# Optimization experiments

Hardware: AMD Instinct MI355X
Metric: run time of the kernel (lower is better)

The kernel has to match this reference:

```python
import jax, jax.numpy as jnp
from jax import lax
import numpy as np

DN = ('NDHWC', 'DHWIO', 'NDHWC')

def _conv(x, W):
    # stride-1 kernel-3 sparse conv on dense grid: SAME conv; absent voxels are zero
    return lax.conv_general_dilated(x, W, (1, 1, 1), 'SAME', dimension_numbers=DN)

def _tconv(x, W):
    # kernel-2 stride-2 generative transpose conv: exactly doubles each spatial dim
    return lax.conv_transpose(x, W, (2, 2, 2), 'VALID', dimension_numbers=DN)

def _pool(h):
    B, D1, D2, D3, C = h.shape
    return h.reshape(B, D1 // 2, 2, D2 // 2, 2, D3 // 2, 2, C).max(axis=(2, 4, 6))

def _pool_mask(m):
    B, D1, D2, D3 = m.shape
    return m.reshape(B, D1 // 2, 2, D2 // 2, 2, D3 // 2, 2).max(axis=(2, 4, 6))

def _up_mask(m):
    return jnp.repeat(jnp.repeat(jnp.repeat(m, 2, axis=1), 2, axis=2), 2, axis=3)

def setup_inputs() -> dict:
    key = jax.random.key(0)
    ks = jax.random.split(key, 6)
    B, G = 2, 128
    x = jax.random.normal(ks[0], (B, G, G, G, 1), dtype=jnp.float32)
    occ = jax.random.randint(ks[1], (B, G, G, G), 0, 10, dtype=jnp.int32)
    def xavier(k, shape):
        fan_in = np.prod(shape[:-1]); fan_out = shape[-1]
        std = np.sqrt(2.0 / (fan_in + fan_out)).astype(np.float32)
        return jax.random.normal(k, shape, dtype=jnp.float32) * std
    W1 = xavier(ks[2], (3, 3, 3, 1, 16))
    W2 = xavier(ks[3], (3, 3, 3, 16, 4))
    Wt1 = xavier(ks[4], (2, 2, 2, 4, 16))
    Wt2 = xavier(ks[5], (2, 2, 2, 16, 1))
    return {"x": x, "W1": W1, "W2": W2, "Wt1": Wt1, "Wt2": Wt2, "occ": occ}

def reference(x, W1, W2, Wt1, Wt2, occ):
    m0 = (occ == 0).astype(x.dtype)            # occupancy mask at full res
    xm = x * m0[..., None]
    h = jax.nn.relu(_conv(xm, W1)) * m0[..., None]   # coords unchanged
    h = _pool(h); m1 = _pool_mask(m0)                # stride-2 max pool on sparse coords
    h = jax.nn.relu(_conv(h, W2)) * m1[..., None]
    h = _pool(h); m2 = _pool_mask(m1)
    m3 = _up_mask(m2)                                # transpose conv emits all children coords
    h = jax.nn.relu(_tconv(h, Wt1)) * m3[..., None]
    m4 = _up_mask(m3)
    out = jax.nn.sigmoid(_tconv(h, Wt2)) * m4[..., None]
    return out
```

## Files before the change

### kernel.cpp

```cpp
#include <hip/hip_runtime.h>
#include <hip/hip_fp16.h>

#define G 128

typedef _Float16 h2_t __attribute__((ext_vector_type(2)));

union U16 { uint4 u; h2_t h2[4]; };
union HV  { uint4 u; h2_t h2[4]; };
union PK2 { uint2 u; h2_t h[2]; };

__device__ __forceinline__ float dot2f(h2_t a, h2_t b, float c) {
#if __has_builtin(__builtin_amdgcn_fdot2)
    return __builtin_amdgcn_fdot2(a, b, c, false);
#else
    return c + (float)a.x * (float)b.x + (float)a.y * (float)b.y;
#endif
}

__device__ __forceinline__ float dot4(float4 a, float4 b) {
    return a.x * b.x + a.y * b.y + a.z * b.z + a.w * b.w;
}

__global__ __launch_bounds__(256, 1)
void k_conv1_pool(const float* __restrict__ x, const int* __restrict__ occ,
                  const float* __restrict__ W1,
                  __half* __restrict__ h1p, float* __restrict__ m1)
{
    __shared__ __align__(16) _Float16      sx[10 * 18 * 24];
    __shared__ __align__(16) int           pacc[16 * 256];
    __shared__ __align__(4)  unsigned short slist[2048];
    __shared__ __align__(16) h2_t          w1L[216];
    __shared__ __align__(4)  unsigned char sm1[256];
    __shared__ int                         scnt;

    const int bx = blockIdx.x, by = blockIdx.y;
    const int b  = blockIdx.z >> 4, zt = blockIdx.z & 15;
    const int tid = threadIdx.x;

    const int z0 = zt * 8 - 1, y0 = by * 16 - 1;
    const int base_b = b * G * G * G;

    int4   ro[5];
    float4 rx[5];
    #pragma unroll
    for (int it = 0; it < 5; ++it) {
        int c = it * 256 + tid;
        int cc = c < 1080 ? c : 1079;
        int row = cc / 6, seg = cc - row * 6;
        int lz  = row / 18, ly = row - lz * 18;
        int gz = z0 + lz, gy = y0 + ly;
        int gxc = (bx << 4) - 4 + (seg << 2);
        bool inb = (unsigned)gz < 128u && (unsigned)gy < 128u && (unsigned)gxc < 128u;
        int gi = inb ? base_b + (gz * G + gy) * G + gxc : base_b;
        ro[it] = *(const int4*)(occ + gi);
        rx[it] = *(const float4*)(x + gi);
    }

    if (tid == 0) scnt = 0;
    {
        uint4 z4 = make_uint4(0u, 0u, 0u, 0u);
        uint4* p4 = (uint4*)pacc;
        p4[tid] = z4; p4[tid + 256] = z4; p4[tid + 512] = z4; p4[tid + 768] = z4;
    }
    if (tid < 64) ((unsigned*)sm1)[tid] = 0u;
    if (tid < 216) {
        float2 f = ((const float2*)W1)[tid];
        h2_t w; w.x = (_Float16)f.x; w.y = (_Float16)f.y;
        w1L[tid] = w;
    }
    __syncthreads();

    #pragma unroll
    for (int it = 0; it < 5; ++it) {
        int c = it * 256 + tid;
        if (c < 1080) {
            int row = c / 6, seg = c - row * 6;
            int lz  = row / 18, ly = row - lz * 18;
            int gz = z0 + lz, gy = y0 + ly;
            int gxc = (bx << 4) - 4 + (seg << 2);
            bool inb = (unsigned)gz < 128u && (unsigned)gy < 128u && (unsigned)gxc < 128u;
            int4   o4 = ro[it];
            float4 x4 = rx[it];
            if (!inb) o4 = make_int4(1, 1, 1, 1);
            h2_t p01, p23;
            p01.x = (o4.x == 0) ? (_Float16)x4.x : (_Float16)0.f;
            p01.y = (o4.y == 0) ? (_Float16)x4.y : (_Float16)0.f;
            p23.x = (o4.z == 0) ? (_Float16)x4.z : (_Float16)0.f;
            p23.y = (o4.w == 0) ? (_Float16)x4.w : (_Float16)0.f;
            PK2 pk; pk.h[0] = p01; pk.h[1] = p23;
            *(uint2*)&sx[row * 24 + (seg << 2)] = pk.u;

            if ((unsigned)(lz - 1) < 8u && (unsigned)(ly - 1) < 16u &&
                (unsigned)(seg - 1) < 4u) {
                int mb = (o4.x == 0 ? 1 : 0) | (o4.y == 0 ? 2 : 0) |
                         (o4.z == 0 ? 4 : 0) | (o4.w == 0 ? 8 : 0);
                if (mb) {
                    int cnt  = __popc(mb);
                    int base = atomicAdd(&scnt, cnt);
                    int cz = lz - 1, cy = ly - 1, cx0v = (seg << 2) - 4;
                    int cellb = (cz >> 1) * 64 + (cy >> 1) * 8;
                    #pragma unroll
                    for (int j = 0; j < 4; ++j) {
                        if (mb & (1 << j)) {
                            slist[base++] = (unsigned short)((cz << 8) | (cy << 4) | (cx0v + j));
                            sm1[cellb + ((cx0v + j) >> 1)] = (unsigned char)1;
                        }
                    }
                }
            }
        }
    }
    __syncthreads();

    const int n = scnt;

    const h2_t zero = (h2_t)(_Float16)0.f;
    for (int kb = 0; kb < n; kb += 256) {
        const int idx = kb + tid;
        if (idx < n) {
            const int code = slist[idx];
            const int cz = code >> 8, cy = (code >> 4) & 15, cx = code & 15;
            const int sb = ((cz + 1) * 18 + (cy + 1)) * 24 + cx + 4;
            h2_t acc[8];
            #pragma unroll
            for (int c = 0; c < 8; ++c) acc[c] = zero;
            #pragma unroll
            for (int kz = 0; kz < 3; ++kz)
            #pragma unroll
            for (int ky = 0; ky < 3; ++ky)
            #pragma unroll
            for (int kx = 0; kx < 3; ++kx) {
                _Float16 v = sx[sb + (kz - 1) * 432 + (ky - 1) * 24 + (kx - 1)];
                h2_t v2 = {v, v};
                const h2_t* w = &w1L[((kz * 3 + ky) * 3 + kx) * 8];
                #pragma unroll
                for (int c = 0; c < 8; ++c) acc[c] = v2 * w[c] + acc[c];
            }
            const int cell = (cz >> 1) * 64 + (cy >> 1) * 8 + (cx >> 1);
            #pragma unroll
            for (int c = 0; c < 8; ++c) {
                atomicMax(&pacc[(2 * c) * 256 + cell],
                          __float_as_int(fmaxf((float)acc[c].x, 0.f)));
                atomicMax(&pacc[(2 * c + 1) * 256 + cell],
                          __float_as_int(fmaxf((float)acc[c].y, 0.f)));
            }
        }
    }
    __syncthreads();

    const int tx = tid & 7, ty = (tid >> 3) & 7, tz = tid >> 6;
    const int pz = zt * 4 + tz, py = by * 8 + ty, px = bx * 8 + tx;
    const int vidx = ((b * 64 + pz) * 64 + py) * 64 + px;
    HV p0, p1;
    #pragma unroll
    for (int c = 0; c < 4; ++c) {
        h2_t a, bq;
        a.x  = (_Float16)__int_as_float(pacc[(2 * c) * 256 + tid]);
        a.y  = (_Float16)__int_as_float(pacc[(2 * c + 1) * 256 + tid]);
        bq.x = (_Float16)__int_as_float(pacc[(8 + 2 * c) * 256 + tid]);
        bq.y = (_Float16)__int_as_float(pacc[(9 + 2 * c) * 256 + tid]);
        p0.h2[c] = a; p1.h2[c] = bq;
    }
    uint4* o = (uint4*)&h1p[(size_t)vidx * 16];
    o[0] = p0.u;
    o[1] = p1.u;
    m1[vidx] = sm1[tid] ? 1.f : 0.f;
}

__global__ __launch_bounds__(256)
void k_conv2_dec(const __half* __restrict__ h1p, const float* __restrict__ m1,
                 const float* __restrict__ W2,
                 const float* __restrict__ Wt1, const float* __restrict__ Wt2,
                 float* __restrict__ out)
{
    __shared__ uint4  tile[1320];
    __shared__ float4 wt1[128];
    __shared__ float4 wt2[32];
    __shared__ __align__(16) h2_t w2L[864];
    __shared__ int    pacc[128];
    __shared__ int    pm[32];
    __shared__ unsigned char slist[256];
    __shared__ int    scnt;

    const int bx = blockIdx.x, by = blockIdx.y;
    const int b  = blockIdx.z >> 4, bz = blockIdx.z & 15;
    const int tid = threadIdx.x;

    const int z0 = bz * 4 - 1, y0 = by * 8 - 1, x0 = bx * 8 - 1;

    uint4 ra[3], rb4[3];
    #pragma unroll
    for (int it = 0; it < 3; ++it) {
        int g = it * 256 + tid;
        int gg = g < 660 ? g : 659;
        int z = gg / 110, r = gg - z * 110, y = r / 11, xx = r - y * 11;
        int gz = z0 + z, gy = y0 + y, gx = x0 + xx;
        bool inb = (unsigned)gz < 64u && (unsigned)gy < 64u && (unsigned)gx < 64u;
        size_t vi = inb ? (size_t)(((b * 64 + gz) * 64 + gy) * 64 + gx) : 0;
        const uint4* src = (const uint4*)&h1p[vi * 16];
        ra[it]  = src[0];
        rb4[it] = src[1];
    }

    const int cx_ = tid & 7, cy_ = (tid >> 3) & 7, cz_ = tid >> 6;
    const float mv = m1[((b * 64 + (bz * 4 + cz_)) * 64 + (by * 8 + cy_)) * 64
                        + (bx * 8 + cx_)];

    if (tid == 0) scnt = 0;
    if (tid < 128) { wt1[tid] = ((const float4*)Wt1)[tid]; pacc[tid] = 0; }
    if (tid < 32)  { wt2[tid] = ((const float4*)Wt2)[tid]; pm[tid] = 0; }
    #pragma unroll
    for (int it = 0; it < 4; ++it) {
        int i = it * 256 + tid;
        if (i < 864) {
            int t = i >> 5, rr = i & 31, co = rr >> 3, p = rr & 7;
            h2_t w;
            w.x = (_Float16)W2[t * 64 + (2 * p) * 4 + co];
            w.y = (_Float16)W2[t * 64 + (2 * p + 1) * 4 + co];
            w2L[i] = w;
        }
    }
    __syncthreads();

    #pragma unroll
    for (int it = 0; it < 3; ++it) {
        int g = it * 256 + tid;
        if (g < 660) {
            int z = g / 110, r = g - z * 110, y = r / 11, xx = r - y * 11;
            int gz = z0 + z, gy = y0 + y, gx = x0 + xx;
            bool inb = (unsigned)gz < 64u && (unsigned)gy < 64u && (unsigned)gx < 64u;
            uint4 a0 = ra[it], a1 = rb4[it];
            if (!inb) { a0 = make_uint4(0u, 0u, 0u, 0u); a1 = a0; }
            tile[g]       = a0;
            tile[660 + g] = a1;
        }
    }
    {
        const int lane = tid & 63;
        bool act = (mv != 0.f);
        unsigned long long bal = __ballot(act);
        int wtot = __popcll(bal);
        int wbase = 0;
        if (lane == 0 && wtot) wbase = atomicAdd(&scnt, wtot);
        wbase = __shfl(wbase, 0);
        if (act) {
            int pre = __popcll(bal & ((1ull << lane) - 1ull));
            slist[wbase + pre] = (unsigned char)tid;
            pm[(cz_ >> 1) * 16 + (cy_ >> 1) * 4 + (cx_ >> 1)] = 1;
        }
    }
    __syncthreads();

    const int n = scnt;

    if (tid < n) {
        const int code = slist[tid];
        const int cx = code & 7, cy = (code >> 3) & 7, cz = code >> 6;
        float acc[4] = {0.f, 0.f, 0.f, 0.f};
        #pragma unroll
        for (int kz = 0; kz < 3; ++kz)
        #pragma unroll
        for (int ky = 0; ky < 3; ++ky) {
            const int rb = ((cz + kz) * 10 + (cy + ky)) * 11 + cx;
            h2_t hp[2][3][4];
            #pragma unroll
            for (int hh = 0; hh < 2; ++hh)
            #pragma unroll
            for (int xi = 0; xi < 3; ++xi) {
                U16 a; a.u = tile[hh * 660 + rb + xi];
                #pragma unroll
                for (int p = 0; p < 4; ++p) hp[hh][xi][p] = a.h2[p];
            }
            const int t3 = (kz * 3 + ky) * 3;
            #pragma unroll
            for (int kx = 0; kx < 3; ++kx) {
                const h2_t* w = &w2L[(t3 + kx) * 32];
                #pragma unroll
                for (int co = 0; co < 4; ++co) {
                    float a = acc[co];
                    #pragma unroll
                    for (int hh = 0; hh < 2; ++hh)
                    #pragma unroll
                    for (int p = 0; p < 4; ++p)
                        a = dot2f(hp[hh][kx][p], w[co * 8 + 4 * hh + p], a);
                    acc[co] = a;
                }
            }
        }
        const int parent = (cz >> 1) * 16 + (cy >> 1) * 4 + (cx >> 1);
        #pragma unroll
        for (int co = 0; co < 4; ++co)
            atomicMax(&pacc[co * 32 + parent],
                      __float_as_int(fmaxf(acc[co], 0.f)));
    }
    __syncthreads();

    {
        const int p  = tid >> 3;
        const int a  = (tid >> 2) & 1;
        const int bb = (tid >> 1) & 1;
        const int e  = tid & 1;
        const int pZ = p >> 4, pY = (p >> 2) & 3, pq = p & 3;
        const int pz = bz * 2 + pZ, py = by * 4 + pY, pxq = bx * 4 + pq;

        const float mm = pm[p] ? 1.f : 0.f;
        const float4 hv = make_float4(__int_as_float(pacc[p]),
                                      __int_as_float(pacc[32 + p]),
                                      __int_as_float(pacc[64 + p]),
                                      __int_as_float(pacc[96 + p]));

        const int b0q = ((((1 - a) * 2 + (1 - bb)) * 2) + 1) * 16;
        const int b1q = ((((1 - a) * 2 + (1 - bb)) * 2) + 0) * 16;
        float4 t0q[4], t1q[4];
        #pragma unroll
        for (int q = 0; q < 4; ++q) {
            float4 a0 = wt1[b0q + q],      a1 = wt1[b0q + 4 + q];
            float4 a2 = wt1[b0q + 8 + q],  a3 = wt1[b0q + 12 + q];
            float4 c0 = wt1[b1q + q],      c1 = wt1[b1q + 4 + q];
            float4 c2 = wt1[b1q + 8 + q],  c3 = wt1[b1q + 12 + q];
            float4 s0, s1;
            s0.x = hv.x * a0.x + hv.y * a1.x + hv.z * a2.x + hv.w * a3.x;
            s0.y = hv.x * a0.y + hv.y * a1.y + hv.z * a2.y + hv.w * a3.y;
            s0.z = hv.x * a0.z + hv.y * a1.z + hv.z * a2.z + hv.w * a3.z;
            s0.w = hv.x * a0.w + hv.y * a1.w + hv.z * a2.w + hv.w * a3.w;
            s1.x = hv.x * c0.x + hv.y * c1.x + hv.z * c2.x + hv.w * c3.x;
            s1.y = hv.x * c0.y + hv.y * c1.y + hv.z * c2.y + hv.w * c3.y;
            s1.z = hv.x * c0.z + hv.y * c1.z + hv.z * c2.z + hv.w * c3.z;
            s1.w = hv.x * c0.w + hv.y * c1.w + hv.z * c2.w + hv.w * c3.w;
            t0q[q] = make_float4(fmaxf(s0.x, 0.f), fmaxf(s0.y, 0.f),
                                 fmaxf(s0.z, 0.f), fmaxf(s0.w, 0.f));
            t1q[q] = make_float4(fmaxf(s1.x, 0.f), fmaxf(s1.y, 0.f),
                                 fmaxf(s1.z, 0.f), fmaxf(s1.w, 0.f));
        }

        const int d = 4 * pz + 2 * a + e;
        #pragma unroll
        for (int f = 0; f < 2; ++f) {
            const int hh = 4 * py + 2 * bb + f;
            const int be = ((1 - e) * 2 + (1 - f)) * 2;
            const float4* wg0 = &wt2[(be + 1) * 4];
            const float4* wg1 = &wt2[(be + 0) * 4];
            float s00 = dot4(t0q[0], wg0[0]) + dot4(t0q[1], wg0[1])
                      + dot4(t0q[2], wg0[2]) + dot4(t0q[3], wg0[3]);
            float s01 = dot4(t0q[0], wg1[0]) + dot4(t0q[1], wg1[1])
                      + dot4(t0q[2], wg1[2]) + dot4(t0q[3], wg1[3]);
            float s10 = dot4(t1q[0], wg0[0]) + dot4(t1q[1], wg0[1])
                      + dot4(t1q[2], wg0[2]) + dot4(t1q[3], wg0[3]);
            float s11 = dot4(t1q[0], wg1[0]) + dot4(t1q[1], wg1[1])
                      + dot4(t1q[2], wg1[2]) + dot4(t1q[3], wg1[3]);
            float4 o;
            o.x = mm / (1.f + __expf(-s00));
            o.y = mm / (1.f + __expf(-s01));
            o.z = mm / (1.f + __expf(-s10));
            o.w = mm / (1.f + __expf(-s11));
            *(float4*)&out[((b * G + d) * G + hh) * G + 4 * pxq] = o;
        }
    }
}

extern "C" void kernel_launch(void* const* d_in, const int* in_sizes, int n_in,
                              void* d_out, int out_size, void* d_ws, size_t ws_size,
                              hipStream_t stream) {
    (void)in_sizes; (void)n_in; (void)out_size; (void)ws_size;
    const float* x   = (const float*)d_in[0];
    const float* W1  = (const float*)d_in[1];
    const float* W2  = (const float*)d_in[2];
    const float* Wt1 = (const float*)d_in[3];
    const float* Wt2 = (const float*)d_in[4];
    const int*   occ = (const int*)d_in[5];
    float* out = (float*)d_out;

    char* ws = (char*)d_ws;
    __half* h1p = (__half*)ws;
    float*  m1  = (float*)(ws + 8388608ull * sizeof(__half));

    k_conv1_pool<<<dim3(8, 8, 32), dim3(256), 0, stream>>>(x, occ, W1, h1p, m1);
    k_conv2_dec<<<dim3(8, 8, 32), dim3(256), 0, stream>>>(h1p, m1, W2, Wt1, Wt2, out);
}
```

Baseline: 152.5 us.

## Halve z-tile per block in both kernels to double grid size

Both kernels now cover half as many z slices per block, so the grid doubles from 2048 to 4096 blocks and shared memory per block shrinks. Conv1 drops the launch-bounds occupancy hint and the register prefetch of occ/x, loading them inline instead. The decoder remaps threads so each one writes a single output row instead of looping over two. The aim is more blocks and higher occupancy to hide latency, at the cost of a larger relative halo overhead (6/4 z rows in conv1, 4/2 in conv2) and half-idle threads in the final write phases.

```diff
diff --git a/kernel.cpp b/kernel.cpp
--- a/kernel.cpp
+++ b/kernel.cpp
@@ -21,48 +21,32 @@
     return a.x * b.x + a.y * b.y + a.z * b.z + a.w * b.w;
 }
 
-__global__ __launch_bounds__(256, 1)
+__global__ __launch_bounds__(256)
 void k_conv1_pool(const float* __restrict__ x, const int* __restrict__ occ,
                   const float* __restrict__ W1,
                   __half* __restrict__ h1p, float* __restrict__ m1)
 {
-    __shared__ __align__(16) _Float16      sx[10 * 18 * 24];
-    __shared__ __align__(16) int           pacc[16 * 256];
-    __shared__ __align__(4)  unsigned short slist[2048];
-    __shared__ __align__(16) h2_t          w1L[216];
-    __shared__ __align__(4)  unsigned char sm1[256];
-    __shared__ int                         scnt;
+    __shared__ __align__(16) _Float16       sx[6 * 18 * 24];
+    __shared__ __align__(16) int            pacc[16 * 128];
+    __shared__ __align__(4)  unsigned short slist[1024];
+    __shared__ __align__(16) h2_t           w1L[216];
+    __shared__ __align__(4)  unsigned char  sm1[128];
+    __shared__ int                          scnt;
 
     const int bx = blockIdx.x, by = blockIdx.y;
-    const int b  = blockIdx.z >> 4, zt = blockIdx.z & 15;
+    const int b  = blockIdx.z >> 5, bz4 = blockIdx.z & 31;
     const int tid = threadIdx.x;
 
-    const int z0 = zt * 8 - 1, y0 = by * 16 - 1;
+    const int z0 = bz4 * 4 - 1, y0 = by * 16 - 1;
     const int base_b = b * G * G * G;
-
-    int4   ro[5];
-    float4 rx[5];
-    #pragma unroll
-    for (int it = 0; it < 5; ++it) {
-        int c = it * 256 + tid;
-        int cc = c < 1080 ? c : 1079;
-        int row = cc / 6, seg = cc - row * 6;
-        int lz  = row / 18, ly = row - lz * 18;
-        int gz = z0 + lz, gy = y0 + ly;
-        int gxc = (bx << 4) - 4 + (seg << 2);
-        bool inb = (unsigned)gz < 128u && (unsigned)gy < 128u && (unsigned)gxc < 128u;
-        int gi = inb ? base_b + (gz * G + gy) * G + gxc : base_b;
-        ro[it] = *(const int4*)(occ + gi);
-        rx[it] = *(const float4*)(x + gi);
-    }
 
     if (tid == 0) scnt = 0;
     {
         uint4 z4 = make_uint4(0u, 0u, 0u, 0u);
-        uint4* p4 = (uint4*)pacc;
-        p4[tid] = z4; p4[tid + 256] = z4; p4[tid + 512] = z4; p4[tid + 768] = z4;
-    }
-    if (tid < 64) ((unsigned*)sm1)[tid] = 0u;
+        ((uint4*)pacc)[tid]       = z4;
+        ((uint4*)pacc)[tid + 256] = z4;
+    }
+    if (tid < 32) ((unsigned*)sm1)[tid] = 0u;
     if (tid < 216) {
         float2 f = ((const float2*)W1)[tid];
         h2_t w; w.x = (_Float16)f.x; w.y = (_Float16)f.y;
@@ -71,16 +55,16 @@
     __syncthreads();
 
     #pragma unroll
-    for (int it = 0; it < 5; ++it) {
+    for (int it = 0; it < 3; ++it) {
         int c = it * 256 + tid;
-        if (c < 1080) {
+        if (c < 648) {
             int row = c / 6, seg = c - row * 6;
-            int lz  = row / 18, ly = row - lz * 18;
-            int gz = z0 + lz, gy = y0 + ly;
-            int gxc = (bx << 4) - 4 + (seg << 2);
+            int lz = row / 18, ly = row - lz * 18;
+            int gz = z0 + lz, gy = y0 + ly, gxc = (bx << 4) - 4 + (seg << 2);
             bool inb = (unsigned)gz < 128u && (unsigned)gy < 128u && (unsigned)gxc < 128u;
-            int4   o4 = ro[it];
-            float4 x4 = rx[it];
+            int gi = inb ? base_b + (gz * G + gy) * G + gxc : base_b;
+            int4   o4 = *(const int4*)(occ + gi);
+            float4 x4 = *(const float4*)(x + gi);
             if (!inb) o4 = make_int4(1, 1, 1, 1);
             h2_t p01, p23;
             p01.x = (o4.x == 0) ? (_Float16)x4.x : (_Float16)0.f;
@@ -90,20 +74,22 @@
             PK2 pk; pk.h[0] = p01; pk.h[1] = p23;
             *(uint2*)&sx[row * 24 + (seg << 2)] = pk.u;
 
-            if ((unsigned)(lz - 1) < 8u && (unsigned)(ly - 1) < 16u &&
-                (unsigned)(seg - 1) < 4u) {
-                int mb = (o4.x == 0 ? 1 : 0) | (o4.y == 0 ? 2 : 0) |
-                         (o4.z == 0 ? 4 : 0) | (o4.w == 0 ? 8 : 0);
+            if ((unsigned)(lz - 1) < 4u && (unsigned)(ly - 1) < 16u) {
+                const int lx0 = seg << 2;
+                int mb = 0;
+                if (o4.x == 0 && (unsigned)(lx0 + 0 - 4) < 16u) mb |= 1;
+                if (o4.y == 0 && (unsigned)(lx0 + 1 - 4) < 16u) mb |= 2;
+                if (o4.z == 0 && (unsigned)(lx0 + 2 - 4) < 16u) mb |= 4;
+                if (o4.w == 0 && (unsigned)(lx0 + 3 - 4) < 16u) mb |= 8;
                 if (mb) {
-                    int cnt  = __popc(mb);
-                    int base = atomicAdd(&scnt, cnt);
-                    int cz = lz - 1, cy = ly - 1, cx0v = (seg << 2) - 4;
-                    int cellb = (cz >> 1) * 64 + (cy >> 1) * 8;
+                    int base = atomicAdd(&scnt, __popc(mb));
+                    const int tb = ((lz - 1) >> 1) * 64 + ((ly - 1) >> 1) * 8;
                     #pragma unroll
                     for (int j = 0; j < 4; ++j) {
                         if (mb & (1 << j)) {
-                            slist[base++] = (unsigned short)((cz << 8) | (cy << 4) | (cx0v + j));
-                            sm1[cellb + ((cx0v + j) >> 1)] = (unsigned char)1;
+                            const int lxv = lx0 + j;
+                            slist[base++] = (unsigned short)((lz << 10) | (ly << 5) | lxv);
+                            sm1[tb + ((lxv - 4) >> 1)] = (unsigned char)1;
                         }
                     }
                 }
@@ -114,57 +100,61 @@
 
     const int n = scnt;
 
-    const h2_t zero = (h2_t)(_Float16)0.f;
-    for (int kb = 0; kb < n; kb += 256) {
-        const int idx = kb + tid;
-        if (idx < n) {
-            const int code = slist[idx];
-            const int cz = code >> 8, cy = (code >> 4) & 15, cx = code & 15;
-            const int sb = ((cz + 1) * 18 + (cy + 1)) * 24 + cx + 4;
-            h2_t acc[8];
-            #pragma unroll
-            for (int c = 0; c < 8; ++c) acc[c] = zero;
-            #pragma unroll
-            for (int kz = 0; kz < 3; ++kz)
-            #pragma unroll
-            for (int ky = 0; ky < 3; ++ky)
-            #pragma unroll
-            for (int kx = 0; kx < 3; ++kx) {
-                _Float16 v = sx[sb + (kz - 1) * 432 + (ky - 1) * 24 + (kx - 1)];
-                h2_t v2 = {v, v};
-                const h2_t* w = &w1L[((kz * 3 + ky) * 3 + kx) * 8];
-                #pragma unroll
-                for (int c = 0; c < 8; ++c) acc[c] = v2 * w[c] + acc[c];
+    {
+        const h2_t zero = (h2_t)(_Float16)0.f;
+        for (int kb = 0; kb < n; kb += 256) {
+            const int idx = kb + tid;
+            if (idx < n) {
+                const int e  = slist[idx];
+                const int lx = e & 31, ly = (e >> 5) & 31, lz = e >> 10;
+                const int sb = (lz * 18 + ly) * 24 + lx;
+                h2_t acc[8];
+                #pragma unroll
+                for (int c = 0; c < 8; ++c) acc[c] = zero;
+                #pragma unroll
+                for (int kz = 0; kz < 3; ++kz)
+                #pragma unroll
+                for (int ky = 0; ky < 3; ++ky)
+                #pragma unroll
+                for (int kx = 0; kx < 3; ++kx) {
+                    _Float16 v = sx[sb + (kz - 1) * 432 + (ky - 1) * 24 + (kx - 1)];
+                    h2_t v2 = {v, v};
+                    const h2_t* w = &w1L[((kz * 3 + ky) * 3 + kx) * 8];
+                    #pragma unroll
+                    for (int c = 0; c < 8; ++c) acc[c] = v2 * w[c] + acc[c];
+                }
+                const int cell = ((lz - 1) >> 1) * 64 + ((ly - 1) >> 1) * 8 + ((lx - 4) >> 1);
+                #pragma unroll
+                for (int c = 0; c < 8; ++c) {
+                    atomicMax(&pacc[(2 * c) * 128 + cell],
+                              __float_as_int(fmaxf((float)acc[c].x, 0.f)));
+                    atomicMax(&pacc[(2 * c + 1) * 128 + cell],
+                              __float_as_int(fmaxf((float)acc[c].y, 0.f)));
+                }
             }
-            const int cell = (cz >> 1) * 64 + (cy >> 1) * 8 + (cx >> 1);
-            #pragma unroll
-            for (int c = 0; c < 8; ++c) {
-                atomicMax(&pacc[(2 * c) * 256 + cell],
-                          __float_as_int(fmaxf((float)acc[c].x, 0.f)));
-                atomicMax(&pacc[(2 * c + 1) * 256 + cell],
-                          __float_as_int(fmaxf((float)acc[c].y, 0.f)));
-            }
-        }
-    }
-    __syncthreads();
-
-    const int tx = tid & 7, ty = (tid >> 3) & 7, tz = tid >> 6;
-    const int pz = zt * 4 + tz, py = by * 8 + ty, px = bx * 8 + tx;
-    const int vidx = ((b * 64 + pz) * 64 + py) * 64 + px;
-    HV p0, p1;
-    #pragma unroll
-    for (int c = 0; c < 4; ++c) {
-        h2_t a, bq;
-        a.x  = (_Float16)__int_as_float(pacc[(2 * c) * 256 + tid]);
-        a.y  = (_Float16)__int_as_float(pacc[(2 * c + 1) * 256 + tid]);
-        bq.x = (_Float16)__int_as_float(pacc[(8 + 2 * c) * 256 + tid]);
-        bq.y = (_Float16)__int_as_float(pacc[(9 + 2 * c) * 256 + tid]);
-        p0.h2[c] = a; p1.h2[c] = bq;
-    }
-    uint4* o = (uint4*)&h1p[(size_t)vidx * 16];
-    o[0] = p0.u;
-    o[1] = p1.u;
-    m1[vidx] = sm1[tid] ? 1.f : 0.f;
+        }
+    }
+    __syncthreads();
+
+    if (tid < 128) {
+        const int tx = tid & 7, ty = (tid >> 3) & 7, tz = tid >> 6;
+        const int pz = bz4 * 2 + tz, py = by * 8 + ty, px = bx * 8 + tx;
+        const int vidx = ((b * 64 + pz) * 64 + py) * 64 + px;
+        HV p0, p1;
+        #pragma unroll
+        for (int c = 0; c < 4; ++c) {
+            h2_t a, bq;
+            a.x  = (_Float16)__int_as_float(pacc[(2 * c) * 128 + tid]);
+            a.y  = (_Float16)__int_as_float(pacc[(2 * c + 1) * 128 + tid]);
+            bq.x = (_Float16)__int_as_float(pacc[(8 + 2 * c) * 128 + tid]);
+            bq.y = (_Float16)__int_as_float(pacc[(9 + 2 * c) * 128 + tid]);
+            p0.h2[c] = a; p1.h2[c] = bq;
+        }
+        uint4* o = (uint4*)&h1p[(size_t)vidx * 16];
+        o[0] = p0.u;
+        o[1] = p1.u;
+        m1[vidx] = sm1[tid] ? 1.f : 0.f;
+    }
 }
 
 __global__ __launch_bounds__(256)
@@ -173,27 +163,27 @@
                  const float* __restrict__ Wt1, const float* __restrict__ Wt2,
                  float* __restrict__ out)
 {
-    __shared__ uint4  tile[1320];
-    __shared__ float4 wt1[128];
-    __shared__ float4 wt2[32];
-    __shared__ __align__(16) h2_t w2L[864];
-    __shared__ int    pacc[128];
-    __shared__ int    pm[32];
-    __shared__ unsigned char slist[256];
-    __shared__ int    scnt;
+    __shared__ __align__(16) uint4 tile[800];
+    __shared__ float4              wt1[128];
+    __shared__ float4              wt2[32];
+    __shared__ __align__(16) h2_t  w2L[864];
+    __shared__ int                 pacc2[64];
+    __shared__ int                 pm[16];
+    __shared__ unsigned char       clist[128];
+    __shared__ int                 scnt;
 
     const int bx = blockIdx.x, by = blockIdx.y;
-    const int b  = blockIdx.z >> 4, bz = blockIdx.z & 15;
+    const int b  = blockIdx.z >> 5, bzq = blockIdx.z & 31;
     const int tid = threadIdx.x;
 
-    const int z0 = bz * 4 - 1, y0 = by * 8 - 1, x0 = bx * 8 - 1;
-
-    uint4 ra[3], rb4[3];
+    const int z0 = bzq * 2 - 1, y0 = by * 8 - 1, x0 = bx * 8 - 1;
+
+    uint4 ra[2], rb4[2];
     #pragma unroll
-    for (int it = 0; it < 3; ++it) {
+    for (int it = 0; it < 2; ++it) {
         int g = it * 256 + tid;
-        int gg = g < 660 ? g : 659;
-        int z = gg / 110, r = gg - z * 110, y = r / 11, xx = r - y * 11;
+        int gg = g < 400 ? g : 399;
+        int z = gg / 100, r = gg - z * 100, y = r / 10, xx = r - y * 10;
         int gz = z0 + z, gy = y0 + y, gx = x0 + xx;
         bool inb = (unsigned)gz < 64u && (unsigned)gy < 64u && (unsigned)gx < 64u;
         size_t vi = inb ? (size_t)(((b * 64 + gz) * 64 + gy) * 64 + gx) : 0;
@@ -202,13 +192,17 @@
         rb4[it] = src[1];
     }
 
-    const int cx_ = tid & 7, cy_ = (tid >> 3) & 7, cz_ = tid >> 6;
-    const float mv = m1[((b * 64 + (bz * 4 + cz_)) * 64 + (by * 8 + cy_)) * 64
-                        + (bx * 8 + cx_)];
+    const int ox_ = tid & 7, oy_ = (tid >> 3) & 7, oz_ = tid >> 6;
+    float mv = 0.f;
+    if (tid < 128)
+        mv = m1[((b * 64 + (bzq * 2 + oz_)) * 64 + (by * 8 + oy_)) * 64
+                + (bx * 8 + ox_)];
 
     if (tid == 0) scnt = 0;
-    if (tid < 128) { wt1[tid] = ((const float4*)Wt1)[tid]; pacc[tid] = 0; }
-    if (tid < 32)  { wt2[tid] = ((const float4*)Wt2)[tid]; pm[tid] = 0; }
+    if (tid < 128) wt1[tid] = ((const float4*)Wt1)[tid];
+    if (tid < 32)  wt2[tid] = ((const float4*)Wt2)[tid];
+    if (tid < 64)  pacc2[tid] = 0;
+    if (tid < 16)  pm[tid] = 0;
     #pragma unroll
     for (int it = 0; it < 4; ++it) {
         int i = it * 256 + tid;
@@ -223,21 +217,21 @@
     __syncthreads();
 
     #pragma unroll
-    for (int it = 0; it < 3; ++it) {
+    for (int it = 0; it < 2; ++it) {
         int g = it * 256 + tid;
-        if (g < 660) {
-            int z = g / 110, r = g - z * 110, y = r / 11, xx = r - y * 11;
+        if (g < 400) {
+            int z = g / 100, r = g - z * 100, y = r / 10, xx = r - y * 10;
             int gz = z0 + z, gy = y0 + y, gx = x0 + xx;
             bool inb = (unsigned)gz < 64u && (unsigned)gy < 64u && (unsigned)gx < 64u;
             uint4 a0 = ra[it], a1 = rb4[it];
             if (!inb) { a0 = make_uint4(0u, 0u, 0u, 0u); a1 = a0; }
             tile[g]       = a0;
-            tile[660 + g] = a1;
+            tile[400 + g] = a1;
         }
     }
     {
         const int lane = tid & 63;
-        bool act = (mv != 0.f);
+        bool act = (tid < 128) && (mv != 0.f);
         unsigned long long bal = __ballot(act);
         int wtot = __popcll(bal);
         int wbase = 0;
@@ -245,8 +239,8 @@
         wbase = __shfl(wbase, 0);
         if (act) {
             int pre = __popcll(bal & ((1ull << lane) - 1ull));
-            slist[wbase + pre] = (unsigned char)tid;
-            pm[(cz_ >> 1) * 16 + (cy_ >> 1) * 4 + (cx_ >> 1)] = 1;
+            clist[wbase + pre] = (unsigned char)tid;
+            pm[(oy_ >> 1) * 4 + (ox_ >> 1)] = 1;
         }
     }
     __syncthreads();
@@ -254,20 +248,20 @@
     const int n = scnt;
 
     if (tid < n) {
-        const int code = slist[tid];
-        const int cx = code & 7, cy = (code >> 3) & 7, cz = code >> 6;
+        const int code = clist[tid];
+        const int ox = code & 7, oy = (code >> 3) & 7, oz = code >> 6;
         float acc[4] = {0.f, 0.f, 0.f, 0.f};
         #pragma unroll
         for (int kz = 0; kz < 3; ++kz)
         #pragma unroll
         for (int ky = 0; ky < 3; ++ky) {
-            const int rb = ((cz + kz) * 10 + (cy + ky)) * 11 + cx;
+            const int rb = ((oz + kz) * 10 + (oy + ky)) * 10 + ox;
             h2_t hp[2][3][4];
             #pragma unroll
             for (int hh = 0; hh < 2; ++hh)
             #pragma unroll
             for (int xi = 0; xi < 3; ++xi) {
-                U16 a; a.u = tile[hh * 660 + rb + xi];
+                U16 a; a.u = tile[hh * 400 + rb + xi];
                 #pragma unroll
                 for (int p = 0; p < 4; ++p) hp[hh][xi][p] = a.h2[p];
             }
@@ -287,27 +281,28 @@
                 }
             }
         }
-        const int parent = (cz >> 1) * 16 + (cy >> 1) * 4 + (cx >> 1);
+        const int parent = (oy >> 1) * 4 + (ox >> 1);
         #pragma unroll
         for (int co = 0; co < 4; ++co)
-            atomicMax(&pacc[co * 32 + parent],
+            atomicMax(&pacc2[co * 16 + parent],
                       __float_as_int(fmaxf(acc[co], 0.f)));
     }
     __syncthreads();
 
     {
-        const int p  = tid >> 3;
-        const int a  = (tid >> 2) & 1;
-        const int bb = (tid >> 1) & 1;
-        const int e  = tid & 1;
-        const int pZ = p >> 4, pY = (p >> 2) & 3, pq = p & 3;
-        const int pz = bz * 2 + pZ, py = by * 4 + pY, pxq = bx * 4 + pq;
+        const int p  = tid >> 4;
+        const int a  = (tid >> 3) & 1;
+        const int bb = (tid >> 2) & 1;
+        const int e  = (tid >> 1) & 1;
+        const int f  = tid & 1;
+        const int pY = p >> 2, pq = p & 3;
+        const int py = by * 4 + pY, pxq = bx * 4 + pq;
 
         const float mm = pm[p] ? 1.f : 0.f;
-        const float4 hv = make_float4(__int_as_float(pacc[p]),
-                                      __int_as_float(pacc[32 + p]),
-                                      __int_as_float(pacc[64 + p]),
-                                      __int_as_float(pacc[96 + p]));
+        const float4 hv = make_float4(__int_as_float(pacc2[p]),
+                                      __int_as_float(pacc2[16 + p]),
+                                      __int_as_float(pacc2[32 + p]),
+                                      __int_as_float(pacc2[48 + p]));
 
         const int b0q = ((((1 - a) * 2 + (1 - bb)) * 2) + 1) * 16;
         const int b1q = ((((1 - a) * 2 + (1 - bb)) * 2) + 0) * 16;
@@ -333,28 +328,25 @@
                                  fmaxf(s1.z, 0.f), fmaxf(s1.w, 0.f));
         }
 
-        const int d = 4 * pz + 2 * a + e;
-        #pragma unroll
-        for (int f = 0; f < 2; ++f) {
-            const int hh = 4 * py + 2 * bb + f;
-            const int be = ((1 - e) * 2 + (1 - f)) * 2;
-            const float4* wg0 = &wt2[(be + 1) * 4];
-            const float4* wg1 = &wt2[(be + 0) * 4];
-            float s00 = dot4(t0q[0], wg0[0]) + dot4(t0q[1], wg0[1])
-                      + dot4(t0q[2], wg0[2]) + dot4(t0q[3], wg0[3]);
-            float s01 = dot4(t0q[0], wg1[0]) + dot4(t0q[1], wg1[1])
-                      + dot4(t0q[2], wg1[2]) + dot4(t0q[3], wg1[3]);
-            float s10 = dot4(t1q[0], wg0[0]) + dot4(t1q[1], wg0[1])
-                      + dot4(t1q[2], wg0[2]) + dot4(t1q[3], wg0[3]);
-            float s11 = dot4(t1q[0], wg1[0]) + dot4(t1q[1], wg1[1])
-                      + dot4(t1q[2], wg1[2]) + dot4(t1q[3], wg1[3]);
-            float4 o;
-            o.x = mm / (1.f + __expf(-s00));
-            o.y = mm / (1.f + __expf(-s01));
-            o.z = mm / (1.f + __expf(-s10));
-            o.w = mm / (1.f + __expf(-s11));
-            *(float4*)&out[((b * G + d) * G + hh) * G + 4 * pxq] = o;
-        }
+        const int d  = 4 * bzq + 2 * a + e;
+        const int hh = 4 * py + 2 * bb + f;
+        const int be = ((1 - e) * 2 + (1 - f)) * 2;
+        const float4* wg0 = &wt2[(be + 1) * 4];
+        const float4* wg1 = &wt2[(be + 0) * 4];
+        float s00 = dot4(t0q[0], wg0[0]) + dot4(t0q[1], wg0[1])
+                  + dot4(t0q[2], wg0[2]) + dot4(t0q[3], wg0[3]);
+        float s01 = dot4(t0q[0], wg1[0]) + dot4(t0q[1], wg1[1])
+                  + dot4(t0q[2], wg1[2]) + dot4(t0q[3], wg1[3]);
+        float s10 = dot4(t1q[0], wg0[0]) + dot4(t1q[1], wg0[1])
+                  + dot4(t1q[2], wg0[2]) + dot4(t1q[3], wg0[3]);
+        float s11 = dot4(t1q[0], wg1[0]) + dot4(t1q[1], wg1[1])
+                  + dot4(t1q[2], wg1[2]) + dot4(t1q[3], wg1[3]);
+        float4 o;
+        o.x = mm / (1.f + __expf(-s00));
+        o.y = mm / (1.f + __expf(-s01));
+        o.z = mm / (1.f + __expf(-s10));
+        o.w = mm / (1.f + __expf(-s11));
+        *(float4*)&out[((b * G + d) * G + hh) * G + 4 * pxq] = o;
     }
 }
 
@@ -374,6 +366,6 @@
     __half* h1p = (__half*)ws;
     float*  m1  = (float*)(ws + 8388608ull * sizeof(__half));
 
-    k_conv1_pool<<<dim3(8, 8, 32), dim3(256), 0, stream>>>(x, occ, W1, h1p, m1);
-    k_conv2_dec<<<dim3(8, 8, 32), dim3(256), 0, stream>>>(h1p, m1, W2, Wt1, Wt2, out);
-}
+    k_conv1_pool<<<dim3(8, 8, 64), dim3(256), 0, stream>>>(x, occ, W1, h1p, m1);
+    k_conv2_dec<<<dim3(8, 8, 64), dim3(256), 0, stream>>>(h1p, m1, W2, Wt1, Wt2, out);
+}
```

Measured after the change: 172.4 us. 1.13x slower.
